# Performance work log

Hardware: AMD Instinct MI355X
Metric: run time of the kernel (lower is better)

Reference implementation:

```python
import jax, jax.numpy as jnp
import numpy as np

N = 2048
IN_FEAT = 256
OUT_FEAT = 64
E_FEAT = 32
NHID = 64
ALPHA = 0.2
NHEADS = 4
NLAYERS = 3
NEG_INF = -9e15


def setup_inputs() -> dict:
    key = jax.random.key(0)
    ks = jax.random.split(key, 6)
    x = jax.random.normal(ks[0], (N, IN_FEAT), dtype=jnp.float32)
    adj = jax.random.randint(ks[1], (N, N), 0, 2, dtype=jnp.int32)
    e = jax.random.normal(ks[2], (N, N, E_FEAT), dtype=jnp.float32)
    # All layers share shapes because in_feat == nhid*nheads and out_feat == nhid.
    # xavier-ish scale
    W_e = jax.random.normal(ks[3], (NLAYERS, NHEADS, E_FEAT, IN_FEAT), dtype=jnp.float32) * (1.414 * (2.0 / (E_FEAT + IN_FEAT)) ** 0.5)
    W = jax.random.normal(ks[4], (NLAYERS, NHEADS, IN_FEAT, NHID), dtype=jnp.float32) * (1.414 * (2.0 / (IN_FEAT + NHID)) ** 0.5)
    a = jax.random.normal(ks[5], (NLAYERS, NHEADS, 3 * NHID), dtype=jnp.float32) * (1.414 * (2.0 / (3 * NHID + 1)) ** 0.5)
    return {"x": x, "adj": adj, "e": e, "W_e": W_e, "W": W, "a": a}


def reference(x, adj, e, W_e, W, a):
    # dropout = 0.0 / eval mode -> identity
    out = W.shape[-1]
    nlayers = W.shape[0]
    mask = (adj > 0)[None]  # [1, N, N], broadcast over heads
    for l in range(nlayers):
        islast = (l == nlayers - 1)
        h = jnp.einsum('ni,hio->hno', x, W[l])  # [H, N, out]
        a1 = a[l, :, :out]            # [H, out]
        a2 = a[l, :, out:2 * out]     # [H, out]
        a3 = a[l, :, 2 * out:]        # [H, out]
        # score_ij = leakyrelu(a1.h_i + a2.h_j + a3.(e_ij @ W_e @ W))
        coef = jnp.einsum('heo,ho->he', jnp.einsum('hei,hio->heo', W_e[l], W[l]), a3)  # [H, E_FEAT]
        e_score = jnp.einsum('nmf,hf->hnm', e, coef)  # [H, N, N]
        s1 = jnp.einsum('hno,ho->hn', h, a1)[:, :, None]
        s2 = jnp.einsum('hno,ho->hn', h, a2)[:, None, :]
        score = jax.nn.leaky_relu(s1 + s2 + e_score, ALPHA)
        att = jax.nn.softmax(jnp.where(mask, score, NEG_INF), axis=-1)
        h_prime = jnp.einsum('hnm,hmo->hno', att, h)  # [H, N, out]
        if islast:
            x = jax.nn.elu(h_prime.mean(axis=0))  # [N, out]
        else:
            # concat heads along feature dim (head-major), with per-head elu
            x = jnp.transpose(jax.nn.elu(h_prime), (1, 0, 2)).reshape(h_prime.shape[1], -1)
    return x
```

## Files before the change

### kernel.cpp

```cpp
#include <hip/hip_runtime.h>
#include <cstdint>
#include <cstddef>

#define Nn 2048
#define FIN 256
#define EFEAT 32
#define HID 64
#define NH 4
#define NL 3
#define LRELU_A 0.2f

typedef _Float16 h4 __attribute__((ext_vector_type(4)));
typedef float f2 __attribute__((ext_vector_type(2)));
typedef float f4 __attribute__((ext_vector_type(4)));

#define NEGH ((_Float16)(-60000.0f))

__global__ void k_coef(const float* __restrict__ W, const float* __restrict__ We,
                       const float* __restrict__ a, float* __restrict__ coef) {
  int lh = blockIdx.x;
  int t = threadIdx.x;
  __shared__ float tl[FIN];
  const float* Wb = W + (size_t)lh * FIN * HID;
  const float* ab = a + (size_t)lh * (3 * HID) + 2 * HID;
  float acc = 0.f;
#pragma unroll 8
  for (int o = 0; o < HID; ++o) acc = fmaf(Wb[(size_t)t * HID + o], ab[o], acc);
  tl[t] = acc;
  __syncthreads();
  if (t < EFEAT) {
    const float* Web = We + ((size_t)lh * EFEAT + t) * FIN;
    float c = 0.f;
    for (int i = 0; i < FIN; ++i) c = fmaf(Web[i], tl[i], c);
    coef[lh * EFEAT + t] = c;
  }
}

template <int C>
__global__ __launch_bounds__(256) void k_escore(
    const float* __restrict__ e, const int* __restrict__ adj,
    const float* __restrict__ coef, _Float16* __restrict__ es) {
  size_t idx = (size_t)blockIdx.x * 256 + threadIdx.x;
  int m = (int)(idx & (Nn - 1));
  int n = (int)(idx >> 11);
  int mt = m >> 6, ml = m & 63;
  const size_t cstride = (size_t)32 * Nn * 64;
  size_t sbase = ((size_t)mt * Nn + n) * 64 + (size_t)ml;
  int aj = adj[idx];
  f2 ev2[16];
  const f4* ep = (const f4*)(e + idx * EFEAT);
#pragma unroll
  for (int g = 0; g < 8; ++g) {
    f4 v = ep[g];
    f2 lo, hi;
    lo[0] = v[0]; lo[1] = v[1];
    hi[0] = v[2]; hi[1] = v[3];
    ev2[g * 2 + 0] = lo;
    ev2[g * 2 + 1] = hi;
  }
#pragma clang loop unroll_count(2)
  for (int c = 0; c < C; ++c) {
    const f2* cf = (const f2*)(coef + c * EFEAT);
    f2 acc2 = {0.f, 0.f};
#pragma unroll
    for (int f = 0; f < 16; ++f) acc2 += ev2[f] * cf[f];
    float acc = acc2[0] + acc2[1];
    es[(size_t)c * cstride + sbase] = aj ? (_Float16)acc : NEGH;
  }
}

__global__ __launch_bounds__(256) void k_h(
    const float* __restrict__ x, const float* __restrict__ W,
    const float* __restrict__ a, int layer,
    _Float16* __restrict__ hT, float* __restrict__ s1, float* __restrict__ s2) {
  int t = threadIdx.x;
  int n0 = blockIdx.x * 4;
  int h = t >> 6, o = t & 63;
  const float* Wb = W + ((size_t)(layer * NH + h) * FIN) * HID + o;
  const float* xb = x + (size_t)n0 * FIN;
  float acc[4] = {};
  for (int i0 = 0; i0 < FIN; i0 += 4) {
    float w0 = Wb[(size_t)(i0 + 0) * HID];
    float w1 = Wb[(size_t)(i0 + 1) * HID];
    float w2 = Wb[(size_t)(i0 + 2) * HID];
    float w3 = Wb[(size_t)(i0 + 3) * HID];
#pragma unroll
    for (int j = 0; j < 4; ++j) {
      float4 xv = *(const float4*)(xb + (size_t)j * FIN + i0);
      acc[j] = fmaf(xv.x, w0, acc[j]);
      acc[j] = fmaf(xv.y, w1, acc[j]);
      acc[j] = fmaf(xv.z, w2, acc[j]);
      acc[j] = fmaf(xv.w, w3, acc[j]);
    }
  }
  const float* ab = a + (size_t)(layer * NH + h) * (3 * HID);
  float a1v = ab[o], a2v = ab[HID + o];
#pragma unroll
  for (int j = 0; j < 4; ++j) {
    float r1 = acc[j] * a1v, r2 = acc[j] * a2v;
#pragma unroll
    for (int d = 1; d < 64; d <<= 1) {
      r1 += __shfl_xor(r1, d, 64);
      r2 += __shfl_xor(r2, d, 64);
    }
    if (o == 0) { s1[h * Nn + n0 + j] = r1; s2[h * Nn + n0 + j] = r2; }
  }
  int mt = n0 >> 6, ml = n0 & 63;
  h4 hv;
#pragma unroll
  for (int j = 0; j < 4; ++j) hv[j] = (_Float16)acc[j];
  *(h4*)(hT + (((size_t)h * 32 + mt) * 64 + o) * 64 + ml) = hv;
}

__global__ __launch_bounds__(512, 2) void k_attn(
    const _Float16* __restrict__ es, const _Float16* __restrict__ hT,
    const float* __restrict__ s1, const float* __restrict__ s2,
    float* __restrict__ hp, float* __restrict__ xn, int layer, int last) {
  int h = blockIdx.x;
  int n0 = blockIdx.y * 16;
  int t = threadIdx.x;
  int w = t >> 6;
  int l = t & 63;
  int col = l & 15, grp = l >> 4;
  int n = n0 + col;
  float s1v = s1[h * Nn + n];
  const _Float16* esb = es + (size_t)(layer * NH + h) * ((size_t)32 * Nn * 64);
  const _Float16* hTb = hT + (size_t)h * ((size_t)32 * 64 * 64);
  const float* s2b = s2 + h * Nn;

  h4 sc16[16];
  float pmax = -3.0e38f;
#pragma unroll
  for (int c16 = 0; c16 < 16; ++c16) {
    int m0 = w * 256 + c16 * 16;
    int mt = m0 >> 6;
    int ml0 = (m0 & 63) + grp * 4;
    h4 ev = *(const h4*)(esb + ((size_t)mt * Nn + n) * 64 + ml0);
    float4 sv = *(const float4*)(s2b + m0 + grp * 4);
    float sc0 = s1v + sv.x + (float)ev[0]; sc0 = fmaxf(sc0, LRELU_A * sc0);
    float sc1 = s1v + sv.y + (float)ev[1]; sc1 = fmaxf(sc1, LRELU_A * sc1);
    float sc2 = s1v + sv.z + (float)ev[2]; sc2 = fmaxf(sc2, LRELU_A * sc2);
    float sc3 = s1v + sv.w + (float)ev[3]; sc3 = fmaxf(sc3, LRELU_A * sc3);
    h4 sch;
    sch[0] = (_Float16)sc0; sch[1] = (_Float16)sc1;
    sch[2] = (_Float16)sc2; sch[3] = (_Float16)sc3;
    sc16[c16] = sch;
    pmax = fmaxf(pmax, fmaxf(fmaxf(sc0, sc1), fmaxf(sc2, sc3)));
  }
  pmax = fmaxf(pmax, __shfl_xor(pmax, 16, 64));
  float M = fmaxf(pmax, __shfl_xor(pmax, 32, 64));

  float S = 0.f;
  f4 acc[4] = {};
#pragma unroll
  for (int c16 = 0; c16 < 16; ++c16) {
    int m0 = w * 256 + c16 * 16;
    int mt = m0 >> 6;
    int ml0 = (m0 & 63) + grp * 4;
    h4 scv = sc16[c16];
    float p0 = __expf((float)scv[0] - M);
    float p1 = __expf((float)scv[1] - M);
    float p2 = __expf((float)scv[2] - M);
    float p3 = __expf((float)scv[3] - M);
    S += p0 + p1 + p2 + p3;
    h4 pb;
    pb[0] = (_Float16)p0; pb[1] = (_Float16)p1;
    pb[2] = (_Float16)p2; pb[3] = (_Float16)p3;
    const _Float16* hp0 = hTb + ((size_t)mt * 64 + col) * 64 + ml0;
#pragma unroll
    for (int ot = 0; ot < 4; ++ot) {
      h4 af = *(const h4*)(hp0 + (size_t)ot * 16 * 64);
      acc[ot] = __builtin_amdgcn_mfma_f32_16x16x16f16(af, pb, acc[ot], 0, 0, 0);
    }
  }
  S += __shfl_xor(S, 16, 64);
  S += __shfl_xor(S, 32, 64);

  __shared__ float red[8][16][64];
  __shared__ float Mw[8][16];
  __shared__ float Sw[8][16];
  if (l < 16) { Mw[w][l] = M; Sw[w][l] = S; }
#pragma unroll
  for (int ot = 0; ot < 4; ++ot)
    *(f4*)&red[w][col][ot * 16 + grp * 4] = acc[ot];
  __syncthreads();

  if (t < 256) {
    int nl = t >> 4, o0 = (t & 15) * 4;
    float Ms = Mw[0][nl];
#pragma unroll
    for (int ww = 1; ww < 8; ++ww) Ms = fmaxf(Ms, Mw[ww][nl]);
    float Ssum = 0.f;
    f4 v = {};
#pragma unroll
    for (int ww = 0; ww < 8; ++ww) {
      float f = __expf(Mw[ww][nl] - Ms);
      Ssum = fmaf(Sw[ww][nl], f, Ssum);
      f4 r = *(const f4*)&red[ww][nl][o0];
      v += r * f;
    }
    float is = 1.0f / Ssum;
    v *= is;
    if (last) {
      *(f4*)(hp + ((size_t)h * Nn + n0 + nl) * HID + o0) = v;
    } else {
      f4 xo;
#pragma unroll
      for (int k = 0; k < 4; ++k) xo[k] = v[k] > 0.f ? v[k] : expm1f(v[k]);
      *(f4*)(xn + (size_t)(n0 + nl) * FIN + h * HID + o0) = xo;
    }
  }
}

__global__ void k_out(const float* __restrict__ hp, float* __restrict__ out) {
  int idx = blockIdx.x * 256 + threadIdx.x;
  int n = idx >> 6, o = idx & 63;
  size_t b = (size_t)n * HID + o;
  float v = 0.25f * (hp[b] + hp[(size_t)Nn * HID + b] +
                     hp[2 * (size_t)Nn * HID + b] + hp[3 * (size_t)Nn * HID + b]);
  out[idx] = v > 0.f ? v : expm1f(v);
}

extern "C" void kernel_launch(void* const* d_in, const int* in_sizes, int n_in,
                              void* d_out, int out_size, void* d_ws, size_t ws_size,
                              hipStream_t stream) {
  const float* x_in = (const float*)d_in[0];
  const int* adj = (const int*)d_in[1];
  const float* e = (const float*)d_in[2];
  const float* We = (const float*)d_in[3];
  const float* W = (const float*)d_in[4];
  const float* a = (const float*)d_in[5];
  float* out = (float*)d_out;

  char* ws = (char*)d_ws;
  size_t off = 0;
  auto alloc = [&](size_t bytes) -> void* {
    off = (off + 255) & ~(size_t)255;
    void* p = ws + off;
    off += bytes;
    return p;
  };
  float* coef = (float*)alloc((size_t)NL * NH * EFEAT * sizeof(float));
  float* s1 = (float*)alloc((size_t)NH * Nn * sizeof(float));
  float* s2 = (float*)alloc((size_t)NH * Nn * sizeof(float));
  float* hp = (float*)alloc((size_t)NH * Nn * HID * sizeof(float));
  float* xA = (float*)alloc((size_t)Nn * FIN * sizeof(float));
  float* xB = (float*)alloc((size_t)Nn * FIN * sizeof(float));
  _Float16* hT = (_Float16*)alloc((size_t)NH * 32 * 64 * 64 * sizeof(_Float16));
  _Float16* es = (_Float16*)alloc((size_t)NL * NH * 32 * Nn * 64 * sizeof(_Float16));

  hipLaunchKernelGGL(k_coef, dim3(NL * NH), dim3(256), 0, stream, W, We, a, coef);

  size_t total = (size_t)Nn * Nn;
  hipLaunchKernelGGL((k_escore<NL * NH>), dim3((unsigned)(total / 256)), dim3(256), 0, stream,
                     e, adj, coef, es);

  for (int l = 0; l < NL; ++l) {
    const float* xcur = (l == 0) ? x_in : ((l == 1) ? xA : xB);
    float* xn = (l == 0) ? xA : xB;
    hipLaunchKernelGGL(k_h, dim3(Nn / 4), dim3(256), 0, stream, xcur, W, a, l, hT, s1, s2);
    hipLaunchKernelGGL(k_attn, dim3(NH, Nn / 16), dim3(512), 0, stream,
                       es, hT, s1, s2, hp, xn, l, l == NL - 1 ? 1 : 0);
  }
  hipLaunchKernelGGL(k_out, dim3(Nn * HID / 256), dim3(256), 0, stream, hp, out);
}
```

Before: 322.9 us.

## Stage edge features through LDS in escore and merge layer-0 h with coef kernel

```diff
diff --git a/kernel.cpp b/kernel.cpp
--- a/kernel.cpp
+++ b/kernel.cpp
@@ -16,11 +16,9 @@
 
 #define NEGH ((_Float16)(-60000.0f))
 
-__global__ void k_coef(const float* __restrict__ W, const float* __restrict__ We,
-                       const float* __restrict__ a, float* __restrict__ coef) {
-  int lh = blockIdx.x;
-  int t = threadIdx.x;
-  __shared__ float tl[FIN];
+__device__ __forceinline__ void coef_body(int lh, int t, const float* __restrict__ W,
+                                          const float* __restrict__ We, const float* __restrict__ a,
+                                          float* __restrict__ coef, float* tl) {
   const float* Wb = W + (size_t)lh * FIN * HID;
   const float* ab = a + (size_t)lh * (3 * HID) + 2 * HID;
   float acc = 0.f;
@@ -36,45 +34,10 @@
   }
 }
 
-template <int C>
-__global__ __launch_bounds__(256) void k_escore(
-    const float* __restrict__ e, const int* __restrict__ adj,
-    const float* __restrict__ coef, _Float16* __restrict__ es) {
-  size_t idx = (size_t)blockIdx.x * 256 + threadIdx.x;
-  int m = (int)(idx & (Nn - 1));
-  int n = (int)(idx >> 11);
-  int mt = m >> 6, ml = m & 63;
-  const size_t cstride = (size_t)32 * Nn * 64;
-  size_t sbase = ((size_t)mt * Nn + n) * 64 + (size_t)ml;
-  int aj = adj[idx];
-  f2 ev2[16];
-  const f4* ep = (const f4*)(e + idx * EFEAT);
-#pragma unroll
-  for (int g = 0; g < 8; ++g) {
-    f4 v = ep[g];
-    f2 lo, hi;
-    lo[0] = v[0]; lo[1] = v[1];
-    hi[0] = v[2]; hi[1] = v[3];
-    ev2[g * 2 + 0] = lo;
-    ev2[g * 2 + 1] = hi;
-  }
-#pragma clang loop unroll_count(2)
-  for (int c = 0; c < C; ++c) {
-    const f2* cf = (const f2*)(coef + c * EFEAT);
-    f2 acc2 = {0.f, 0.f};
-#pragma unroll
-    for (int f = 0; f < 16; ++f) acc2 += ev2[f] * cf[f];
-    float acc = acc2[0] + acc2[1];
-    es[(size_t)c * cstride + sbase] = aj ? (_Float16)acc : NEGH;
-  }
-}
-
-__global__ __launch_bounds__(256) void k_h(
-    const float* __restrict__ x, const float* __restrict__ W,
-    const float* __restrict__ a, int layer,
-    _Float16* __restrict__ hT, float* __restrict__ s1, float* __restrict__ s2) {
-  int t = threadIdx.x;
-  int n0 = blockIdx.x * 4;
+__device__ __forceinline__ void h_body(int n0, int t, const float* __restrict__ x,
+                                       const float* __restrict__ W, const float* __restrict__ a,
+                                       int layer, _Float16* __restrict__ hT,
+                                       float* __restrict__ s1, float* __restrict__ s2) {
   int h = t >> 6, o = t & 63;
   const float* Wb = W + ((size_t)(layer * NH + h) * FIN) * HID + o;
   const float* xb = x + (size_t)n0 * FIN;
@@ -110,6 +73,70 @@
 #pragma unroll
   for (int j = 0; j < 4; ++j) hv[j] = (_Float16)acc[j];
   *(h4*)(hT + (((size_t)h * 32 + mt) * 64 + o) * 64 + ml) = hv;
+}
+
+__global__ __launch_bounds__(256) void k_h0_coef(
+    const float* __restrict__ x, const float* __restrict__ W, const float* __restrict__ We,
+    const float* __restrict__ a, _Float16* __restrict__ hT,
+    float* __restrict__ s1, float* __restrict__ s2, float* __restrict__ coef) {
+  __shared__ float tl[FIN];
+  if (blockIdx.x < Nn / 4) {
+    h_body(blockIdx.x * 4, threadIdx.x, x, W, a, 0, hT, s1, s2);
+  } else {
+    coef_body(blockIdx.x - Nn / 4, threadIdx.x, W, We, a, coef, tl);
+  }
+}
+
+__global__ __launch_bounds__(256) void k_h(
+    const float* __restrict__ x, const float* __restrict__ W,
+    const float* __restrict__ a, int layer,
+    _Float16* __restrict__ hT, float* __restrict__ s1, float* __restrict__ s2) {
+  h_body(blockIdx.x * 4, threadIdx.x, x, W, a, layer, hT, s1, s2);
+}
+
+template <int C>
+__global__ __launch_bounds__(256) void k_escore(
+    const float* __restrict__ e, const int* __restrict__ adj,
+    const float* __restrict__ coef, _Float16* __restrict__ es) {
+  __shared__ float se[256 * 34];
+  int t = threadIdx.x;
+  size_t base = (size_t)blockIdx.x * 256;
+  const f4* src = (const f4*)(e + base * EFEAT);
+#pragma unroll
+  for (int k = 0; k < 8; ++k) {
+    int j = t + 256 * k;
+    f4 v = src[j];
+    int r = j >> 3, c = j & 7;
+    float* dst = &se[r * 34 + c * 4];
+    f2 lo, hi;
+    lo[0] = v[0]; lo[1] = v[1]; hi[0] = v[2]; hi[1] = v[3];
+    *(f2*)dst = lo;
+    *(f2*)(dst + 2) = hi;
+  }
+  __syncthreads();
+  size_t idx = base + t;
+  int m = (int)(idx & (Nn - 1));
+  int n = (int)(idx >> 11);
+  int mt = m >> 6, ml = m & 63;
+  const size_t cstride = (size_t)32 * Nn * 64;
+  size_t sbase = ((size_t)mt * Nn + n) * 64 + (size_t)ml;
+  int aj = adj[idx];
+  f2 ev2[16];
+  const float* myrow = &se[t * 34];
+#pragma unroll
+  for (int g = 0; g < 8; ++g) {
+    ev2[2 * g + 0] = *(const f2*)(myrow + g * 4);
+    ev2[2 * g + 1] = *(const f2*)(myrow + g * 4 + 2);
+  }
+#pragma clang loop unroll_count(2)
+  for (int c = 0; c < C; ++c) {
+    const f2* cf = (const f2*)(coef + c * EFEAT);
+    f2 acc2 = {0.f, 0.f};
+#pragma unroll
+    for (int f = 0; f < 16; ++f) acc2 += ev2[f] * cf[f];
+    float acc = acc2[0] + acc2[1];
+    es[(size_t)c * cstride + sbase] = aj ? (_Float16)acc : NEGH;
+  }
 }
 
 __global__ __launch_bounds__(512, 2) void k_attn(
@@ -249,16 +276,19 @@
   _Float16* hT = (_Float16*)alloc((size_t)NH * 32 * 64 * 64 * sizeof(_Float16));
   _Float16* es = (_Float16*)alloc((size_t)NL * NH * 32 * Nn * 64 * sizeof(_Float16));
 
-  hipLaunchKernelGGL(k_coef, dim3(NL * NH), dim3(256), 0, stream, W, We, a, coef);
+  hipLaunchKernelGGL(k_h0_coef, dim3(Nn / 4 + NL * NH), dim3(256), 0, stream,
+                     x_in, W, We, a, hT, s1, s2, coef);
 
   size_t total = (size_t)Nn * Nn;
   hipLaunchKernelGGL((k_escore<NL * NH>), dim3((unsigned)(total / 256)), dim3(256), 0, stream,
                      e, adj, coef, es);
 
   for (int l = 0; l < NL; ++l) {
-    const float* xcur = (l == 0) ? x_in : ((l == 1) ? xA : xB);
+    if (l > 0) {
+      const float* xcur = (l == 1) ? xA : xB;
+      hipLaunchKernelGGL(k_h, dim3(Nn / 4), dim3(256), 0, stream, xcur, W, a, l, hT, s1, s2);
+    }
     float* xn = (l == 0) ? xA : xB;
-    hipLaunchKernelGGL(k_h, dim3(Nn / 4), dim3(256), 0, stream, xcur, W, a, l, hT, s1, s2);
     hipLaunchKernelGGL(k_attn, dim3(NH, Nn / 16), dim3(512), 0, stream,
                        es, hT, s1, s2, hp, xn, l, l == NL - 1 ? 1 : 0);
   }
```

Result: faster. 315.4 us (-2.3%).
